# Kernel tuning notes

Measured on AMD Instinct MI355X. Metric: run time of the kernel, lower is better.

## Reference

```python
import jax, jax.numpy as jnp
import numpy as np
import math

B, T, E, H = 8, 1024, 768, 12
D = E // H  # 64

def setup_inputs() -> dict:
    key = jax.random.key(0)
    ks = jax.random.split(key, 5)
    return {
        "x": jax.random.normal(ks[0], (B, T, E), dtype=jnp.float32),
        "w_attn": jax.random.normal(ks[1], (E, 3 * E), dtype=jnp.float32) * 0.02,
        "b_attn": jax.random.normal(ks[2], (3 * E,), dtype=jnp.float32) * 0.02,
        "w_proj": jax.random.normal(ks[3], (E, E), dtype=jnp.float32) * 0.02,
        "b_proj": jax.random.normal(ks[4], (E,), dtype=jnp.float32) * 0.02,
    }

def reference(x, w_attn, b_attn, w_proj, b_proj):
    b, t, e = x.shape
    h, d = H, E // H
    qkv = x @ w_attn + b_attn                      # [B,T,3E]
    q, k, v = jnp.split(qkv, 3, axis=2)
    q = q.reshape(b, t, h, d).transpose(0, 2, 1, 3)  # [B,H,T,D]
    k = k.reshape(b, t, h, d).transpose(0, 2, 1, 3)
    v = v.reshape(b, t, h, d).transpose(0, 2, 1, 3)
    scores = jnp.einsum('bhqd,bhkd->bhqk', q, k)     # [B,H,T,T]
    causal = jnp.tril(jnp.ones((t, t), dtype=bool))
    scores = jnp.where(causal[None, None], scores, -jnp.inf)
    attn = jax.nn.softmax(scores / jnp.float32(math.sqrt(d)), axis=-1)
    out = jnp.einsum('bhqk,bhkd->bhqd', attn, v)     # [B,H,T,D]
    out = out.transpose(0, 2, 1, 3).reshape(b, t, h * d)
    return out @ w_proj + b_proj
```

## Files before the change

### kernel.cpp

```cpp
#include <hip/hip_runtime.h>
#include <math.h>


#define B_ 8
#define T_ 1024
#define E_ 768
#define H_ 12
#define D_ 64
#define E3 (3 * E_)

typedef __attribute__((ext_vector_type(8))) short bf16x8;
typedef __attribute__((ext_vector_type(4))) float f32x4;

#define SCALE 0.18033688f

__device__ __forceinline__ unsigned short f2bf(float f) {
    unsigned int u = __builtin_bit_cast(unsigned int, f);
    u += 0x7fffu + ((u >> 16) & 1u);
    return (unsigned short)(u >> 16);
}

__device__ __forceinline__ void async_copy16(void* lds, const void* g) {
    __builtin_amdgcn_global_load_lds(
        (const __attribute__((address_space(1))) void*)g,
        (__attribute__((address_space(3))) void*)lds, 16, 0, 0);
}

#define NCVT 6144
#define NTA  (72 * 24)
#define NTP  (24 * 24)

__device__ __forceinline__ void transpose_tile(
    const float* __restrict__ W, unsigned short* __restrict__ Wt,
    int K, int N, int gx, int gy, unsigned short (*tile)[33])
{
    const int n0 = gx * 32, k0 = gy * 32;
    const int tx = threadIdx.x & 31, ty = threadIdx.x >> 5;
    #pragma unroll
    for (int i = 0; i < 4; ++i)
        tile[ty + i * 8][tx] = f2bf(W[(size_t)(k0 + ty + i * 8) * N + n0 + tx]);
    __syncthreads();
    #pragma unroll
    for (int i = 0; i < 4; ++i)
        Wt[(size_t)(n0 + ty + i * 8) * K + k0 + tx] = tile[tx][ty + i * 8];
}

__global__ __launch_bounds__(256) void prep_kernel(
    const float* __restrict__ x, unsigned short* __restrict__ x_bf,
    const float* __restrict__ w_attn, unsigned short* __restrict__ wat,
    const float* __restrict__ w_proj, unsigned short* __restrict__ wpt)
{
    __shared__ unsigned short tile[32][33];
    const int bid = blockIdx.x;
    if (bid < NCVT) {
        const int i = bid * 256 + threadIdx.x;
        float4 f = ((const float4*)x)[i];
        ushort4 o;
        o.x = f2bf(f.x); o.y = f2bf(f.y); o.z = f2bf(f.z); o.w = f2bf(f.w);
        ((ushort4*)x_bf)[i] = o;
    } else if (bid < NCVT + NTA) {
        const int t = bid - NCVT;
        transpose_tile(w_attn, wat, E_, E3, t % 72, t / 72, tile);
    } else {
        const int t = bid - NCVT - NTA;
        transpose_tile(w_proj, wpt, E_, E_, t % 24, t / 24, tile);
    }
}

__global__ __launch_bounds__(512, 2) void gemm_qkv_256(
    const unsigned short* __restrict__ A,
    const unsigned short* __restrict__ Wt,
    const float* __restrict__ bias,
    unsigned short* __restrict__ C,
    unsigned short* __restrict__ vt)
{
    constexpr int K = 768;
    constexpr int N = E3;
    constexpr int NI = 6;

    extern __shared__ unsigned short lds[];
    unsigned short* const Ab0 = lds;
    unsigned short* const Ab1 = lds + 16384;
    unsigned short* const Bb0 = lds + 32768;
    unsigned short* const Bb1 = lds + 49152;

    const int tid  = threadIdx.x;
    const int lane = tid & 63;
    const int w    = tid >> 6;
    const int wm   = w >> 2;
    const int wn   = w & 3;
    const int n16  = lane & 15;
    const int quad = lane >> 4;
    const int l7   = lane & 7;
    const int lrow = lane >> 3;
    const int lcol = (l7 ^ lrow) * 8;

    const int lin  = blockIdx.x;
    const int work = (lin & 7) * 36 + (lin >> 3);
    const int by = work / 9, bx = work % 9;
    const int bm = by * 256, bn = bx * 256;

    const unsigned short* Asrc = A  + (size_t)(bm + w * 16 + lrow) * K + lcol;
    const unsigned short* Bsrc = Wt + (size_t)(bn + w * 16 + lrow) * K + lcol;

    auto stgA = [&](unsigned short* buf, int kt, int h) {
        #pragma unroll
        for (int i = 0; i < 2; ++i)
            async_copy16(&buf[h * 8192 + (w * 2 + i) * 512],
                         Asrc + (size_t)(h * 128 + i * 8) * K + kt * 64);
    };
    auto stgB = [&](unsigned short* buf, int kt, int h) {
        #pragma unroll
        for (int i = 0; i < 2; ++i)
            async_copy16(&buf[h * 8192 + (w * 2 + i) * 512],
                         Bsrc + (size_t)(h * 128 + i * 8) * K + kt * 64);
    };

    bf16x8 afr[8], b0f[4], b1f[4];
    f32x4 acc[8][4] = {};

#define LDA(buf, qm) { \
    _Pragma("unroll") \
    for (int ml = 0; ml < 4; ++ml) { \
        const int r = wm * 16 + ((qm) * 4 + ml) * 32 + n16; \
        const unsigned short* rp = (buf) + r * 64; \
        afr[ml * 2 + 0] = *(const bf16x8*)&rp[((0 + quad) ^ l7) * 8]; \
        afr[ml * 2 + 1] = *(const bf16x8*)&rp[((4 + quad) ^ l7) * 8]; \
    } }
#define LDB(bfr, buf, qn) { \
    _Pragma("unroll") \
    for (int nl = 0; nl < 2; ++nl) { \
        const int r = wn * 16 + ((qn) * 2 + nl) * 64 + n16; \
        const unsigned short* rp = (buf) + r * 64; \
        bfr[nl * 2 + 0] = *(const bf16x8*)&rp[((0 + quad) ^ l7) * 8]; \
        bfr[nl * 2 + 1] = *(const bf16x8*)&rp[((4 + quad) ^ l7) * 8]; \
    } }
#define MM(qm, qn, bfr) { \
    _Pragma("unroll") \
    for (int ml = 0; ml < 4; ++ml) \
    _Pragma("unroll") \
    for (int nl = 0; nl < 2; ++nl) \
    _Pragma("unroll") \
    for (int kk = 0; kk < 2; ++kk) \
        acc[(qm) * 4 + ml][(qn) * 2 + nl] = __builtin_amdgcn_mfma_f32_16x16x32_bf16( \
            afr[ml * 2 + kk], bfr[nl * 2 + kk], acc[(qm) * 4 + ml][(qn) * 2 + nl], 0, 0, 0); }

#define BARR  __builtin_amdgcn_s_barrier()
#define LGKM0 asm volatile("s_waitcnt lgkmcnt(0)" ::: "memory")
#define VM6   asm volatile("s_waitcnt vmcnt(6)" ::: "memory")
#define VM0   asm volatile("s_waitcnt vmcnt(0)" ::: "memory")
#define PRI1  __builtin_amdgcn_s_setprio(1)
#define PRI0  __builtin_amdgcn_s_setprio(0)

    stgA(Ab0, 0, 0); stgB(Bb0, 0, 0); stgB(Bb0, 0, 1); stgA(Ab0, 0, 1);
    stgA(Ab1, 1, 0); stgB(Bb1, 1, 0); stgB(Bb1, 1, 1);
    VM6; BARR;

    #pragma unroll 1
    for (int I = 0; I < NI - 1; ++I) {
        const int u = 2 * I;
        LDA(Ab0, 0); LDB(b0f, Bb0, 0);
        stgA(Ab1, u + 1, 1);
        BARR; LGKM0; PRI1; MM(0, 0, b0f); PRI0; BARR;
        LDB(b1f, Bb0, 1);
        stgA(Ab0, u + 2, 0);
        BARR; LGKM0; PRI1; MM(0, 1, b1f); PRI0; BARR;
        LDA(Ab0, 1);
        stgB(Bb0, u + 2, 0);
        BARR; LGKM0; PRI1; MM(1, 1, b1f); PRI0; BARR;
        stgB(Bb0, u + 2, 1);
        BARR; LGKM0; PRI1; MM(1, 0, b0f); PRI0; VM6; BARR;
        LDA(Ab1, 0); LDB(b0f, Bb1, 0);
        stgA(Ab0, u + 2, 1);
        BARR; LGKM0; PRI1; MM(0, 0, b0f); PRI0; BARR;
        LDB(b1f, Bb1, 1);
        stgA(Ab1, u + 3, 0);
        BARR; LGKM0; PRI1; MM(0, 1, b1f); PRI0; BARR;
        LDA(Ab1, 1);
        stgB(Bb1, u + 3, 0);
        BARR; LGKM0; PRI1; MM(1, 1, b1f); PRI0; BARR;
        stgB(Bb1, u + 3, 1);
        BARR; LGKM0; PRI1; MM(1, 0, b0f); PRI0; VM6; BARR;
    }

    LDA(Ab0, 0); LDB(b0f, Bb0, 0);
    stgA(Ab1, 11, 1);
    BARR; LGKM0; PRI1; MM(0, 0, b0f); PRI0; BARR;
    LDB(b1f, Bb0, 1);
    BARR; LGKM0; PRI1; MM(0, 1, b1f); PRI0; BARR;
    LDA(Ab0, 1);
    BARR; LGKM0; PRI1; MM(1, 1, b1f); PRI0; BARR;
    BARR; PRI1; MM(1, 0, b0f); PRI0; VM0; BARR;
    LDA(Ab1, 0); LDB(b0f, Bb1, 0);
    BARR; LGKM0; PRI1; MM(0, 0, b0f); PRI0; BARR;
    LDB(b1f, Bb1, 1);
    BARR; LGKM0; PRI1; MM(0, 1, b1f); PRI0; BARR;
    LDA(Ab1, 1);
    BARR; LGKM0; PRI1; MM(1, 1, b1f); PRI0; BARR;
    PRI1; MM(1, 0, b0f); PRI0;

#undef LDA
#undef LDB
#undef MM

    if (bx >= 6) {
        #pragma unroll
        for (int m = 0; m < 8; ++m) {
            const int tt = bm + wm * 16 + m * 32 + quad * 4;
            const size_t bb = (size_t)(tt >> 10) * 768;
            const int tin = tt & 1023;
            #pragma unroll
            for (int n = 0; n < 4; ++n) {
                const int col = bn + wn * 16 + n * 64 + n16;
                const int ch = col - 1536;
                const float bv = bias[col];
                ushort4 o4;
                o4.x = f2bf(acc[m][n][0] + bv);
                o4.y = f2bf(acc[m][n][1] + bv);
                o4.z = f2bf(acc[m][n][2] + bv);
                o4.w = f2bf(acc[m][n][3] + bv);
                *(ushort4*)&vt[(bb + ch) * 1024 + tin] = o4;
            }
        }
    } else {
        const bool scale_q = bx < 3;
        #pragma unroll
        for (int m = 0; m < 8; ++m) {
            #pragma unroll
            for (int r = 0; r < 4; ++r) {
                const size_t rowoff = (size_t)(bm + wm * 16 + m * 32 + quad * 4 + r) * N;
                #pragma unroll
                for (int n = 0; n < 4; ++n) {
                    const int col = bn + wn * 16 + n * 64 + n16;
                    float v = acc[m][n][r] + bias[col];
                    if (scale_q) v *= SCALE;
                    C[rowoff + col] = f2bf(v);
                }
            }
        }
    }
}

template <typename OutT, int MODE, int BM, int BN, int WR, int WC>
__global__ __launch_bounds__(256) void gemm_mfma_kernel(
    const unsigned short* __restrict__ A,
    const unsigned short* __restrict__ Wt,
    const float* __restrict__ bias,
    OutT* __restrict__ C,
    unsigned short* __restrict__ vt,
    int M, int N, int K)
{
    constexpr int MT = BM / WR / 16;
    constexpr int NT = BN / WC / 16;
    constexpr int CA = BM / 32;
    constexpr int CB = BN / 32;
    constexpr int QBX = 768 / BN;
    constexpr int VBX = 1536 / BN;

    __shared__ unsigned short Abuf[BM * 64];
    __shared__ unsigned short Bbuf[BN * 64];

    const int tid = threadIdx.x;
    const int lane = tid & 63;
    const int w = tid >> 6;
    const int n16 = lane & 15;
    const int quad = lane >> 4;

    const int nbx = gridDim.x;
    const int lin = blockIdx.y * nbx + blockIdx.x;
    const int band_sz = 8 * nbx;
    const int band = lin / band_sz;
    const int rr = lin % band_sz;
    const int bm = (band * 8 + (rr & 7)) * BM;
    const int bx = rr >> 3;
    const int bn = bx * BN;

    const int wmbase = (w / WC) * (BM / WR);
    const int wnbase = (w % WC) * (BN / WC);

    const int lrow = lane >> 3;
    const int lcol = ((lane & 7) ^ lrow) * 8;

    f32x4 acc[MT][NT] = {};

    for (int k0 = 0; k0 < K; k0 += 64) {
        __syncthreads();
        #pragma unroll
        for (int i = 0; i < CA; ++i) {
            const int c = w * CA + i;
            const int row = c * 8 + lrow;
            async_copy16(&Abuf[c * 512], A + (size_t)(bm + row) * K + k0 + lcol);
        }
        #pragma unroll
        for (int i = 0; i < CB; ++i) {
            const int c = w * CB + i;
            const int row = c * 8 + lrow;
            async_copy16(&Bbuf[c * 512], Wt + (size_t)(bn + row) * K + k0 + lcol);
        }
        __syncthreads();

        #pragma unroll
        for (int kc = 0; kc < 2; ++kc) {
            bf16x8 af[MT], bf[NT];
            #pragma unroll
            for (int mt = 0; mt < MT; ++mt) {
                const int r = wmbase + mt * 16 + n16;
                af[mt] = *(const bf16x8*)&Abuf[r * 64 + ((kc * 4 + quad) ^ (r & 7)) * 8];
            }
            #pragma unroll
            for (int nt = 0; nt < NT; ++nt) {
                const int r = wnbase + nt * 16 + n16;
                bf[nt] = *(const bf16x8*)&Bbuf[r * 64 + ((kc * 4 + quad) ^ (r & 7)) * 8];
            }
            #pragma unroll
            for (int mt = 0; mt < MT; ++mt)
                #pragma unroll
                for (int nt = 0; nt < NT; ++nt)
                    acc[mt][nt] = __builtin_amdgcn_mfma_f32_16x16x32_bf16(
                        af[mt], bf[nt], acc[mt][nt], 0, 0, 0);
        }
    }

    if (MODE == 1 && bx >= VBX) {
        #pragma unroll
        for (int mt = 0; mt < MT; ++mt) {
            const int tt = bm + wmbase + mt * 16 + quad * 4;
            const size_t bb = (size_t)(tt >> 10) * 768;
            const int tin = tt & 1023;
            #pragma unroll
            for (int nt = 0; nt < NT; ++nt) {
                const int col = bn + wnbase + nt * 16 + n16;
                const int ch = col - 1536;
                const float bv = bias[col];
                ushort4 o4;
                o4.x = f2bf(acc[mt][nt][0] + bv);
                o4.y = f2bf(acc[mt][nt][1] + bv);
                o4.z = f2bf(acc[mt][nt][2] + bv);
                o4.w = f2bf(acc[mt][nt][3] + bv);
                *(ushort4*)&vt[(bb + ch) * 1024 + tin] = o4;
            }
        }
        return;
    }

    const bool scale_q = (MODE == 1) && (bx < QBX);
    #pragma unroll
    for (int mt = 0; mt < MT; ++mt) {
        #pragma unroll
        for (int r = 0; r < 4; ++r) {
            const size_t rowoff = (size_t)(bm + wmbase + mt * 16 + quad * 4 + r) * N;
            #pragma unroll
            for (int nt = 0; nt < NT; ++nt) {
                const int col = bn + wnbase + nt * 16 + n16;
                float v = acc[mt][nt][r] + bias[col];
                if (scale_q) v *= SCALE;
                if constexpr (sizeof(OutT) == 2) C[rowoff + col] = (OutT)f2bf(v);
                else                             C[rowoff + col] = (OutT)v;
            }
        }
    }
}

#define BKEY 128

__global__ __launch_bounds__(256, 3) void flash_attn_kernel(
    const unsigned short* __restrict__ qkv,
    const unsigned short* __restrict__ vt,
    unsigned short* __restrict__ out)
{
    __shared__ __align__(16) unsigned short Ks[2][BKEY * 64];
    __shared__ __align__(16) unsigned short Vts[64 * BKEY];

    const int tid = threadIdx.x;
    const int idx = blockIdx.x;
    const int xcd = idx & 7;
    const int j   = idx >> 3;
    const int head = xcd * 12 + (j % 12);
    const int p    = j / 12;
    const int h = head % H_;
    const int b = head / H_;

    const int lane = tid & 63;
    const int w    = tid >> 6;
    const int n16  = lane & 15;
    const int quad = lane >> 4;

    const size_t base = (size_t)b * T_ * E3;
    const unsigned short* qbase = qkv + base + h * D_;
    const unsigned short* kbase = qkv + base + E_ + h * D_;
    const unsigned short* vtb   = vt + (size_t)(b * H_ + h) * 64 * 1024;

    const int lrow = lane >> 3;
    const int lcol = ((lane & 7) ^ lrow) * 8;
    const int vr4 = lane >> 4;
    const int vc  = lane & 15;

    const int qtA = p, qtB = 15 - p;
    const int nIterA = (qtA + 2) >> 1;
    const int nIterB = (qtB + 2) >> 1;
    const int wqA = qtA * 64 + w * 16;
    const int wqB = qtB * 64 + w * 16;

    const unsigned short* qrpA = qbase + (size_t)(wqA + n16) * E3 + quad * 8;
    bf16x8 qfA0 = *(const bf16x8*)qrpA;
    bf16x8 qfA1 = *(const bf16x8*)(qrpA + 32);
    const unsigned short* qrpB = qbase + (size_t)(wqB + n16) * E3 + quad * 8;
    bf16x8 qfB0 = *(const bf16x8*)qrpB;
    bf16x8 qfB1 = *(const bf16x8*)(qrpB + 32);

    f32x4 oA[4] = {}, oB[4] = {};
    float lsA = 0.f, lsB = 0.f;

    const int sLo = n16 + 32 * (quad & 1);
    const int sHi = sLo + 16;
    const bool hiSel = quad >= 2;

    auto stageK = [&](int t) {
        unsigned short* dst = Ks[t & 1];
        const int k0 = t * BKEY;
        #pragma unroll
        for (int i = 0; i < 4; ++i) {
            const int c = w * 4 + i;
            const int row = c * 8 + lrow;
            async_copy16(&dst[c * 512], kbase + (size_t)(k0 + row) * E3 + lcol);
        }
    };
    auto stageV = [&](int t) {
        const int k0 = t * BKEY;
        #pragma unroll
        for (int i = 0; i < 4; ++i) {
            const int jj = w * 4 + i;
            const int row = 4 * jj + vr4;
            async_copy16(&Vts[4 * jj * BKEY],
                         vtb + (size_t)row * 1024 + k0 + ((vc ^ (row & 15)) * 8));
        }
    };

    auto phase = [&](bf16x8 qf0, bf16x8 qf1, f32x4* o, float& lsum,
                     int wave_q_min, int k0, const unsigned short* Kb,
                     bool doMid, bool notLast) {
        int knt_lim = ((wave_q_min + 15 - k0) >> 4) + 1;
        if (knt_lim > 8) knt_lim = 8;
        const int ks_lim = (knt_lim + 1) >> 1;
        const int nkp = ks_lim * 2;
        int Ab2 = wave_q_min - k0 - 15;
        int kfull = Ab2 < 0 ? 0 : (Ab2 >> 4) + 1;
        if (kfull > 8) kfull = 8;

        const int qcol = wave_q_min + n16;

        f32x4 s[8];
        #pragma unroll
        for (int knt = 0; knt < 8; ++knt) {
            if (knt < knt_lim) {
                const int r = knt * 16 + n16;
                bf16x8 kf0 = *(const bf16x8*)&Kb[r * 64 + ((0 + quad) ^ (r & 7)) * 8];
                bf16x8 kf1 = *(const bf16x8*)&Kb[r * 64 + ((4 + quad) ^ (r & 7)) * 8];
                f32x4 acc = {0.f, 0.f, 0.f, 0.f};
                acc = __builtin_amdgcn_mfma_f32_16x16x32_bf16(kf0, qf0, acc, 0, 0, 0);
                acc = __builtin_amdgcn_mfma_f32_16x16x32_bf16(kf1, qf1, acc, 0, 0, 0);
                s[knt] = acc;
            }
        }
        #pragma unroll
        for (int knt = 0; knt < 8; ++knt) {
            if (knt >= kfull && knt < nkp) {
                const int krow = k0 + knt * 16 + quad * 4;
                #pragma unroll
                for (int r = 0; r < 4; ++r) {
                    float v = (knt < knt_lim) ? s[knt][r] : -1e30f;
                    if (krow + r > qcol) v = -1e30f;
                    s[knt][r] = v;
                }
            }
        }

        unsigned int e0[8], e1[8];
        #pragma unroll
        for (int knt = 0; knt < 8; ++knt) {
            if (knt < nkp) {
                float pv0 = __builtin_amdgcn_exp2f(s[knt][0]);
                float pv1 = __builtin_amdgcn_exp2f(s[knt][1]);
                float pv2 = __builtin_amdgcn_exp2f(s[knt][2]);
                float pv3 = __builtin_amdgcn_exp2f(s[knt][3]);
                lsum += (pv0 + pv1) + (pv2 + pv3);
                unsigned int u0 = __builtin_bit_cast(unsigned int, pv0);
                unsigned int u1 = __builtin_bit_cast(unsigned int, pv1);
                unsigned int u2 = __builtin_bit_cast(unsigned int, pv2);
                unsigned int u3 = __builtin_bit_cast(unsigned int, pv3);
                e0[knt] = ((u0 + 0x8000u) >> 16) | ((u1 + 0x8000u) & 0xffff0000u);
                e1[knt] = ((u2 + 0x8000u) >> 16) | ((u3 + 0x8000u) & 0xffff0000u);
            }
        }

        if (doMid) {
            if (notLast) asm volatile("s_waitcnt vmcnt(4)" ::: "memory");
            else         asm volatile("s_waitcnt vmcnt(0)" ::: "memory");
            __builtin_amdgcn_s_barrier();
        }

        #pragma unroll
        for (int ks = 0; ks < 4; ++ks) {
            if (ks < ks_lim) {
                const int kA = 2 * ks, kB = 2 * ks + 1;
                unsigned int a0 = (unsigned)__shfl((int)e0[kA], sLo);
                unsigned int a1 = (unsigned)__shfl((int)e1[kA], sLo);
                unsigned int a2 = (unsigned)__shfl((int)e0[kA], sHi);
                unsigned int a3 = (unsigned)__shfl((int)e1[kA], sHi);
                unsigned int b0 = (unsigned)__shfl((int)e0[kB], sLo);
                unsigned int b1 = (unsigned)__shfl((int)e1[kB], sLo);
                unsigned int b2 = (unsigned)__shfl((int)e0[kB], sHi);
                unsigned int b3 = (unsigned)__shfl((int)e1[kB], sHi);
                uint4 pu;
                pu.x = hiSel ? b0 : a0;
                pu.y = hiSel ? b1 : a1;
                pu.z = hiSel ? b2 : a2;
                pu.w = hiSel ? b3 : a3;
                bf16x8 pf = __builtin_bit_cast(bf16x8, pu);
                #pragma unroll
                for (int dt = 0; dt < 4; ++dt) {
                    const int row = dt * 16 + n16;
                    bf16x8 vf = *(const bf16x8*)&Vts[row * BKEY +
                                    (((ks * 4 + quad) ^ n16) * 8)];
                    o[dt] = __builtin_amdgcn_mfma_f32_16x16x32_bf16(pf, vf, o[dt], 0, 0, 0);
                }
            }
        }
    };

    stageK(0);
    asm volatile("s_waitcnt vmcnt(0)" ::: "memory");
    __builtin_amdgcn_s_barrier();

    for (int it = 0; it < nIterB; ++it) {
        const int k0 = it * BKEY;
        const bool notLast = (it + 1 < nIterB);

        stageV(it);
        if (notLast) stageK(it + 1);
        const unsigned short* Kb = Ks[it & 1];

        phase(qfB0, qfB1, oB, lsB, wqB, k0, Kb, true,  notLast);
        if (it < nIterA)
            phase(qfA0, qfA1, oA, lsA, wqA, k0, Kb, false, notLast);

        asm volatile("s_waitcnt vmcnt(0)" ::: "memory");
        __builtin_amdgcn_s_barrier();
    }

    lsA += __shfl_xor(lsA, 16); lsA += __shfl_xor(lsA, 32);
    lsB += __shfl_xor(lsB, 16); lsB += __shfl_xor(lsB, 32);

    #pragma unroll
    for (int r = 0; r < 4; ++r) {
        const float invA = 1.f / __shfl(lsA, quad * 4 + r);
        unsigned short* orowA = out + ((size_t)b * T_ + wqA + quad * 4 + r) * E_ + h * D_;
        #pragma unroll
        for (int dt = 0; dt < 4; ++dt)
            orowA[dt * 16 + n16] = f2bf(oA[dt][r] * invA);
        const float invB = 1.f / __shfl(lsB, quad * 4 + r);
        unsigned short* orowB = out + ((size_t)b * T_ + wqB + quad * 4 + r) * E_ + h * D_;
        #pragma unroll
        for (int dt = 0; dt < 4; ++dt)
            orowB[dt * 16 + n16] = f2bf(oB[dt][r] * invB);
    }
}

extern "C" void kernel_launch(void* const* d_in, const int* in_sizes, int n_in,
                              void* d_out, int out_size, void* d_ws, size_t ws_size,
                              hipStream_t stream)
{
    const float* x      = (const float*)d_in[0];
    const float* w_attn = (const float*)d_in[1];
    const float* b_attn = (const float*)d_in[2];
    const float* w_proj = (const float*)d_in[3];
    const float* b_proj = (const float*)d_in[4];
    float* out = (float*)d_out;

    const int M = B_ * T_;

    unsigned short* x_bf   = (unsigned short*)d_ws;
    unsigned short* wat    = x_bf + (size_t)M * E_;
    unsigned short* wpt    = wat + (size_t)E3 * E_;
    unsigned short* qkv_bf = wpt + (size_t)E_ * E_;
    unsigned short* att_bf = qkv_bf + (size_t)M * E3;
    unsigned short* vt_bf  = att_bf + (size_t)M * E_;

    static bool qkv_attr_set = false;
    if (!qkv_attr_set) {
        hipFuncSetAttribute((const void*)gemm_qkv_256,
                            hipFuncAttributeMaxDynamicSharedMemorySize, 131072);
        qkv_attr_set = true;
    }

    prep_kernel<<<NCVT + NTA + NTP, 256, 0, stream>>>(x, x_bf, w_attn, wat, w_proj, wpt);

    gemm_qkv_256<<<dim3(288), dim3(512), 131072, stream>>>(
        x_bf, wat, b_attn, qkv_bf, vt_bf);

    flash_attn_kernel<<<B_ * H_ * 8, 256, 0, stream>>>(qkv_bf, vt_bf, att_bf);

    gemm_mfma_kernel<float, 0, 64, 128, 2, 2>
        <<<dim3(E_ / 128, M / 64), 256, 0, stream>>>(
        att_bf, wpt, b_proj, out, nullptr, M, E_, E_);
}
```

Baseline: 186.5 us.

## Retile QKV GEMM to 128x192 blocks with simpler double-buffered loop

Replaces the 256x256-tile QKV GEMM, which used a hand-scheduled 8-phase pipeline, with a 128x192 tile kernel launched on 768 blocks. The new kernel uses a plain double-buffered K loop with one barrier pair per K-step, and cuts LDS so more blocks fit per CU. The goal is to fill all CUs better than 288 large blocks do (the wave-quantization cost) while keeping the async global-to-LDS copies. In exchange each tile reuses less data, there is more global traffic per flop, and the fine-grained overlap of LDS reads with MFMA is gone.

Measured after the change: 167.2 us. 10.3% less time.

```diff
diff --git a/kernel.cpp b/kernel.cpp
--- a/kernel.cpp
+++ b/kernel.cpp
@@ -67,7 +67,8 @@
     }
 }
 
-__global__ __launch_bounds__(512, 2) void gemm_qkv_256(
+
+__global__ __launch_bounds__(512, 4) void gemm_qkv_128x192(
     const unsigned short* __restrict__ A,
     const unsigned short* __restrict__ Wt,
     const float* __restrict__ bias,
@@ -76,13 +77,9 @@
 {
     constexpr int K = 768;
     constexpr int N = E3;
-    constexpr int NI = 6;
+    constexpr int NKT = 12;
 
     extern __shared__ unsigned short lds[];
-    unsigned short* const Ab0 = lds;
-    unsigned short* const Ab1 = lds + 16384;
-    unsigned short* const Bb0 = lds + 32768;
-    unsigned short* const Bb1 = lds + 49152;
 
     const int tid  = threadIdx.x;
     const int lane = tid & 63;
@@ -96,121 +93,88 @@
     const int lcol = (l7 ^ lrow) * 8;
 
     const int lin  = blockIdx.x;
-    const int work = (lin & 7) * 36 + (lin >> 3);
-    const int by = work / 9, bx = work % 9;
-    const int bm = by * 256, bn = bx * 256;
-
-    const unsigned short* Asrc = A  + (size_t)(bm + w * 16 + lrow) * K + lcol;
-    const unsigned short* Bsrc = Wt + (size_t)(bn + w * 16 + lrow) * K + lcol;
-
-    auto stgA = [&](unsigned short* buf, int kt, int h) {
-        #pragma unroll
-        for (int i = 0; i < 2; ++i)
-            async_copy16(&buf[h * 8192 + (w * 2 + i) * 512],
-                         Asrc + (size_t)(h * 128 + i * 8) * K + kt * 64);
+    const int s    = lin >> 3;
+    const int by   = (lin & 7) * 8 + s / 12;
+    const int bx   = s % 12;
+    const int bm = by * 128, bn = bx * 192;
+
+    const unsigned short* Asrc = A  + (size_t)(bm + lrow) * K + lcol;
+    const unsigned short* Bsrc = Wt + (size_t)(bn + lrow) * K + lcol;
+
+    auto stage = [&](int bi, int kt) {
+        unsigned short* ab = lds + (bi ? 8192 : 0);
+        unsigned short* bb = lds + 16384 + (bi ? 12288 : 0);
+        #pragma unroll
+        for (int i = 0; i < 2; ++i) {
+            const int c = w * 2 + i;
+            async_copy16(&ab[c * 512], Asrc + (size_t)(c * 8) * K + kt * 64);
+        }
+        #pragma unroll
+        for (int i = 0; i < 3; ++i) {
+            const int c = w * 3 + i;
+            async_copy16(&bb[c * 512], Bsrc + (size_t)(c * 8) * K + kt * 64);
+        }
     };
-    auto stgB = [&](unsigned short* buf, int kt, int h) {
-        #pragma unroll
-        for (int i = 0; i < 2; ++i)
-            async_copy16(&buf[h * 8192 + (w * 2 + i) * 512],
-                         Bsrc + (size_t)(h * 128 + i * 8) * K + kt * 64);
-    };
-
-    bf16x8 afr[8], b0f[4], b1f[4];
-    f32x4 acc[8][4] = {};
-
-#define LDA(buf, qm) { \
-    _Pragma("unroll") \
-    for (int ml = 0; ml < 4; ++ml) { \
-        const int r = wm * 16 + ((qm) * 4 + ml) * 32 + n16; \
-        const unsigned short* rp = (buf) + r * 64; \
-        afr[ml * 2 + 0] = *(const bf16x8*)&rp[((0 + quad) ^ l7) * 8]; \
-        afr[ml * 2 + 1] = *(const bf16x8*)&rp[((4 + quad) ^ l7) * 8]; \
-    } }
-#define LDB(bfr, buf, qn) { \
-    _Pragma("unroll") \
-    for (int nl = 0; nl < 2; ++nl) { \
-        const int r = wn * 16 + ((qn) * 2 + nl) * 64 + n16; \
-        const unsigned short* rp = (buf) + r * 64; \
-        bfr[nl * 2 + 0] = *(const bf16x8*)&rp[((0 + quad) ^ l7) * 8]; \
-        bfr[nl * 2 + 1] = *(const bf16x8*)&rp[((4 + quad) ^ l7) * 8]; \
-    } }
-#define MM(qm, qn, bfr) { \
-    _Pragma("unroll") \
-    for (int ml = 0; ml < 4; ++ml) \
-    _Pragma("unroll") \
-    for (int nl = 0; nl < 2; ++nl) \
-    _Pragma("unroll") \
-    for (int kk = 0; kk < 2; ++kk) \
-        acc[(qm) * 4 + ml][(qn) * 2 + nl] = __builtin_amdgcn_mfma_f32_16x16x32_bf16( \
-            afr[ml * 2 + kk], bfr[nl * 2 + kk], acc[(qm) * 4 + ml][(qn) * 2 + nl], 0, 0, 0); }
+
+    f32x4 acc[4][3] = {};
 
 #define BARR  __builtin_amdgcn_s_barrier()
-#define LGKM0 asm volatile("s_waitcnt lgkmcnt(0)" ::: "memory")
-#define VM6   asm volatile("s_waitcnt vmcnt(6)" ::: "memory")
+#define VM5   asm volatile("s_waitcnt vmcnt(5)" ::: "memory")
 #define VM0   asm volatile("s_waitcnt vmcnt(0)" ::: "memory")
 #define PRI1  __builtin_amdgcn_s_setprio(1)
 #define PRI0  __builtin_amdgcn_s_setprio(0)
 
-    stgA(Ab0, 0, 0); stgB(Bb0, 0, 0); stgB(Bb0, 0, 1); stgA(Ab0, 0, 1);
-    stgA(Ab1, 1, 0); stgB(Bb1, 1, 0); stgB(Bb1, 1, 1);
-    VM6; BARR;
+    stage(0, 0);
 
     #pragma unroll 1
-    for (int I = 0; I < NI - 1; ++I) {
-        const int u = 2 * I;
-        LDA(Ab0, 0); LDB(b0f, Bb0, 0);
-        stgA(Ab1, u + 1, 1);
-        BARR; LGKM0; PRI1; MM(0, 0, b0f); PRI0; BARR;
-        LDB(b1f, Bb0, 1);
-        stgA(Ab0, u + 2, 0);
-        BARR; LGKM0; PRI1; MM(0, 1, b1f); PRI0; BARR;
-        LDA(Ab0, 1);
-        stgB(Bb0, u + 2, 0);
-        BARR; LGKM0; PRI1; MM(1, 1, b1f); PRI0; BARR;
-        stgB(Bb0, u + 2, 1);
-        BARR; LGKM0; PRI1; MM(1, 0, b0f); PRI0; VM6; BARR;
-        LDA(Ab1, 0); LDB(b0f, Bb1, 0);
-        stgA(Ab0, u + 2, 1);
-        BARR; LGKM0; PRI1; MM(0, 0, b0f); PRI0; BARR;
-        LDB(b1f, Bb1, 1);
-        stgA(Ab1, u + 3, 0);
-        BARR; LGKM0; PRI1; MM(0, 1, b1f); PRI0; BARR;
-        LDA(Ab1, 1);
-        stgB(Bb1, u + 3, 0);
-        BARR; LGKM0; PRI1; MM(1, 1, b1f); PRI0; BARR;
-        stgB(Bb1, u + 3, 1);
-        BARR; LGKM0; PRI1; MM(1, 0, b0f); PRI0; VM6; BARR;
-    }
-
-    LDA(Ab0, 0); LDB(b0f, Bb0, 0);
-    stgA(Ab1, 11, 1);
-    BARR; LGKM0; PRI1; MM(0, 0, b0f); PRI0; BARR;
-    LDB(b1f, Bb0, 1);
-    BARR; LGKM0; PRI1; MM(0, 1, b1f); PRI0; BARR;
-    LDA(Ab0, 1);
-    BARR; LGKM0; PRI1; MM(1, 1, b1f); PRI0; BARR;
-    BARR; PRI1; MM(1, 0, b0f); PRI0; VM0; BARR;
-    LDA(Ab1, 0); LDB(b0f, Bb1, 0);
-    BARR; LGKM0; PRI1; MM(0, 0, b0f); PRI0; BARR;
-    LDB(b1f, Bb1, 1);
-    BARR; LGKM0; PRI1; MM(0, 1, b1f); PRI0; BARR;
-    LDA(Ab1, 1);
-    BARR; LGKM0; PRI1; MM(1, 1, b1f); PRI0; BARR;
-    PRI1; MM(1, 0, b0f); PRI0;
-
-#undef LDA
-#undef LDB
-#undef MM
-
-    if (bx >= 6) {
-        #pragma unroll
-        for (int m = 0; m < 8; ++m) {
+    for (int u = 0; u < NKT; ++u) {
+        const int bi = u & 1;
+        const unsigned short* ab = lds + (bi ? 8192 : 0);
+        const unsigned short* bb = lds + 16384 + (bi ? 12288 : 0);
+        if (u < NKT - 1) {
+            stage(bi ^ 1, u + 1);
+            VM5;
+        } else {
+            VM0;
+        }
+        BARR;
+
+        #pragma unroll
+        for (int kc = 0; kc < 2; ++kc) {
+            bf16x8 af[4], bf[3];
+            #pragma unroll
+            for (int m = 0; m < 4; ++m) {
+                const int r = wm * 16 + m * 32 + n16;
+                af[m] = *(const bf16x8*)&ab[r * 64 + (((kc * 4 + quad) ^ (r & 7)) * 8)];
+            }
+            #pragma unroll
+            for (int n = 0; n < 3; ++n) {
+                const int r = wn * 16 + n * 64 + n16;
+                bf[n] = *(const bf16x8*)&bb[r * 64 + (((kc * 4 + quad) ^ (r & 7)) * 8)];
+            }
+            PRI1;
+            #pragma unroll
+            for (int m = 0; m < 4; ++m)
+                #pragma unroll
+                for (int n = 0; n < 3; ++n)
+                    acc[m][n] = __builtin_amdgcn_mfma_f32_16x16x32_bf16(
+                        af[m], bf[n], acc[m][n], 0, 0, 0);
+            PRI0;
+        }
+        BARR;
+    }
+
+#undef VM5
+#undef VM0
+
+    if (bx >= 8) {
+        #pragma unroll
+        for (int m = 0; m < 4; ++m) {
             const int tt = bm + wm * 16 + m * 32 + quad * 4;
-            const size_t bb = (size_t)(tt >> 10) * 768;
+            const size_t bb2 = (size_t)(tt >> 10) * 768;
             const int tin = tt & 1023;
             #pragma unroll
-            for (int n = 0; n < 4; ++n) {
+            for (int n = 0; n < 3; ++n) {
                 const int col = bn + wn * 16 + n * 64 + n16;
                 const int ch = col - 1536;
                 const float bv = bias[col];
@@ -219,18 +183,18 @@
                 o4.y = f2bf(acc[m][n][1] + bv);
                 o4.z = f2bf(acc[m][n][2] + bv);
                 o4.w = f2bf(acc[m][n][3] + bv);
-                *(ushort4*)&vt[(bb + ch) * 1024 + tin] = o4;
+                *(ushort4*)&vt[(bb2 + ch) * 1024 + tin] = o4;
             }
         }
     } else {
-        const bool scale_q = bx < 3;
-        #pragma unroll
-        for (int m = 0; m < 8; ++m) {
+        const bool scale_q = bx < 4;
+        #pragma unroll
+        for (int m = 0; m < 4; ++m) {
             #pragma unroll
             for (int r = 0; r < 4; ++r) {
                 const size_t rowoff = (size_t)(bm + wm * 16 + m * 32 + quad * 4 + r) * N;
                 #pragma unroll
-                for (int n = 0; n < 4; ++n) {
+                for (int n = 0; n < 3; ++n) {
                     const int col = bn + wn * 16 + n * 64 + n16;
                     float v = acc[m][n][r] + bias[col];
                     if (scale_q) v *= SCALE;
@@ -588,14 +552,14 @@
 
     static bool qkv_attr_set = false;
     if (!qkv_attr_set) {
-        hipFuncSetAttribute((const void*)gemm_qkv_256,
-                            hipFuncAttributeMaxDynamicSharedMemorySize, 131072);
+        (void)hipFuncSetAttribute((const void*)gemm_qkv_128x192,
+                                  hipFuncAttributeMaxDynamicSharedMemorySize, 81920);
         qkv_attr_set = true;
     }
 
     prep_kernel<<<NCVT + NTA + NTP, 256, 0, stream>>>(x, x_bf, w_attn, wat, w_proj, wpt);
 
-    gemm_qkv_256<<<dim3(288), dim3(512), 131072, stream>>>(
+    gemm_qkv_128x192<<<dim3(768), dim3(512), 81920, stream>>>(
         x_bf, wat, b_attn, qkv_bf, vt_bf);
 
     flash_attn_kernel<<<B_ * H_ * 8, 256, 0, stream>>>(qkv_bf, vt_bf, att_bf);
```
